# Optimization experiments

Hardware: AMD Instinct MI355X
Metric: run time of the kernel (lower is better)

The kernel has to match this reference:

```python
import jax, jax.numpy as jnp
import numpy as np

NW1, L1 = 4096, 36
NW2, L2 = 1024, 100
D, NHEAD = 128, 8
HD = D // NHEAD
# alternating full / half-full windows -> exact token count
N1 = (NW1 // 2) * (L1 + L1 // 2)   # 110592
N2 = (NW2 // 2) * (L2 + L2 // 2)   # 76800
N = N1 + N2                        # 187392


def _build_group(nw, L, perm, start):
    """Prefix-valid windows: even windows full (L tokens), odd half (L//2)."""
    lens = np.where(np.arange(nw) % 2 == 0, L, L // 2)
    valid = np.arange(L)[None, :] < lens[:, None]          # [nw, L]
    inds = np.zeros((nw, L), np.int32)
    n = int(lens.sum())
    inds[valid] = perm[start:start + n]                    # row-major prefix fill
    return inds, ~valid, start + n


def setup_inputs() -> dict:
    rng = np.random.default_rng(0)
    perm = rng.permutation(N).astype(np.int32)
    inds1, mask1, ptr = _build_group(NW1, L1, perm, 0)
    inds2, mask2, ptr = _build_group(NW2, L2, perm, ptr)
    assert ptr == N
    ks = jax.random.split(jax.random.key(0), 7)
    scale = 1.0 / np.sqrt(D)
    return {
        "feat_2d": jax.random.normal(ks[0], (N, D), jnp.float32),
        "pos1": jax.random.normal(ks[1], (NW1, L1, D), jnp.float32),
        "pos2": jax.random.normal(ks[2], (NW2, L2, D), jnp.float32),
        "in_proj_w": jax.random.normal(ks[3], (3 * D, D), jnp.float32) * scale,
        "in_proj_b": jax.random.normal(ks[4], (3 * D,), jnp.float32) * 0.02,
        "out_proj_w": jax.random.normal(ks[5], (D, D), jnp.float32) * scale,
        "out_proj_b": jax.random.normal(ks[6], (D,), jnp.float32) * 0.02,
        "inds1": jnp.asarray(inds1),
        "inds2": jnp.asarray(inds2),
        "mask1": jnp.asarray(mask1),
        "mask2": jnp.asarray(mask2),
    }


def _mha(qk, v, pad_mask, Wi, bi, Wo, bo):
    """torch.nn.MultiheadAttention math (eval mode, dropout=0).
    qk, v: [nw, L, D]; pad_mask: [nw, L] True=padded key."""
    nw, L, _ = qk.shape
    q = (qk @ Wi[:D].T + bi[:D]).reshape(nw, L, NHEAD, HD)
    k = (qk @ Wi[D:2 * D].T + bi[D:2 * D]).reshape(nw, L, NHEAD, HD)
    vv = (v @ Wi[2 * D:].T + bi[2 * D:]).reshape(nw, L, NHEAD, HD)
    scores = jnp.einsum('nqhd,nkhd->nhqk', q, k) * (HD ** -0.5)
    scores = jnp.where(pad_mask[:, None, None, :],
                       jnp.finfo(scores.dtype).min, scores)
    attn = jax.nn.softmax(scores, axis=-1)
    out = jnp.einsum('nhqk,nkhd->nqhd', attn, vv).reshape(nw, L, D)
    return out @ Wo.T + bo


def reference(feat_2d, pos1, pos2, in_proj_w, in_proj_b, out_proj_w,
              out_proj_b, inds1, inds2, mask1, mask2):
    out = jnp.zeros_like(feat_2d)
    for inds, mask, pos in ((inds1, mask1, pos1), (inds2, mask2, pos2)):
        f = feat_2d[inds]                      # flat2window gather [nw, L, D]
        o = _mha(f + pos, f, mask,
                 in_proj_w, in_proj_b, out_proj_w, out_proj_b)
        o = o * (~mask)[..., None]             # zero padded slots
        out = out.at[inds.reshape(-1)].add(o.reshape(-1, D))  # window2flat
    return out
```

## Files before the change

### kernel.cpp

```cpp
#include <hip/hip_runtime.h>

typedef __attribute__((ext_vector_type(4))) float f32x4;
typedef __attribute__((ext_vector_type(8))) short short8;
typedef __attribute__((ext_vector_type(4))) short short4v;

#define MFMA_B16(a,b,c) __builtin_amdgcn_mfma_f32_16x16x32_bf16((a),(b),(c),0,0,0)

static __device__ __forceinline__ unsigned short f2bf(float x){
  unsigned int u = __float_as_uint(x);
  u += 0x7fffu + ((u >> 16) & 1u);
  return (unsigned short)(u >> 16);
}

static __device__ __forceinline__ short8 pack8(f32x4 a, f32x4 b){
  short8 r;
  r[0]=(short)f2bf(a[0]); r[1]=(short)f2bf(a[1]); r[2]=(short)f2bf(a[2]); r[3]=(short)f2bf(a[3]);
  r[4]=(short)f2bf(b[0]); r[5]=(short)f2bf(b[1]); r[6]=(short)f2bf(b[2]); r[7]=(short)f2bf(b[3]);
  return r;
}

static __device__ __forceinline__ short4v pack4(const f32x4& a){
  short4v r;
  r[0]=(short)f2bf(a[0]); r[1]=(short)f2bf(a[1]); r[2]=(short)f2bf(a[2]); r[3]=(short)f2bf(a[3]);
  return r;
}

__global__ void prep_w(const float* __restrict__ ipw, const float* __restrict__ opw,
                       unsigned short* __restrict__ wbf){
  int i = blockIdx.x * 256 + threadIdx.x;
  float v = (i < 384*128) ? ipw[i] : opw[i - 384*128];
  wbf[i] = f2bf(v);
}

#define STR 136

#define PSTR2 (16*8 + 8)
#define STRT2 24
#define KOFF2 (16*7)

#define TT3 3
#define PSTR3 (16*(TT3+1) + 8)
#define STRT3 24
#define KOFF3 (16*TT3)
#define HALF3 (2*48*STR + 4*16*PSTR3 + 4*16*STRT3)

__global__ __launch_bounds__(512, 4)
void fused_all(const float* __restrict__ feat,
               const float* __restrict__ pos1, const float* __restrict__ pos2,
               const int* __restrict__ inds1, const int* __restrict__ inds2,
               const unsigned short* __restrict__ wqkv,
               const unsigned short* __restrict__ wout,
               const float* __restrict__ ipb, const float* __restrict__ opb,
               float* __restrict__ out)
{
  extern __shared__ __align__(16) unsigned short smem[];
  const int b  = blockIdx.x;
  const int tid = threadIdx.x;
  const short8 Z8 = {0,0,0,0,0,0,0,0};
  const f32x4  Z4 = {0.f,0.f,0.f,0.f};

  if (b < 1024){
    unsigned short* sQK = smem;
    unsigned short* sF  = smem + 112*STR;
    unsigned short* sPb = smem + 2*112*STR;
    unsigned short* sTs = sPb + 4*16*PSTR2;

    const int w  = b;
    const int Lv = (w & 1) ? 50 : 100;
    const int T  = (Lv + 15) >> 4;
    const long ibase = (long)w * 100;
    const int wv4 = tid >> 6, lane = tid & 63, c = lane & 15, q = lane >> 4;

    {
      const int rg = tid >> 4, ch = tid & 15;
      #pragma unroll
      for (int s = 0; s < 4; ++s){
        const int row = s*32 + rg;
        if (row < 16*T){
          short8 fv = Z8, qv = Z8;
          if (row < Lv){
            const int tok = inds2[ibase + row];
            const float* fr = feat + (long)tok*128 + ch*8;
            const float* pr = pos2 + (ibase + row)*128 + ch*8;
            f32x4 f0 = *(const f32x4*)fr, f1 = *(const f32x4*)(fr+4);
            f32x4 p0 = *(const f32x4*)pr, p1 = *(const f32x4*)(pr+4);
            fv = pack8(f0, f1); qv = pack8(f0+p0, f1+p1);
          }
          *(short8*)&sF [row*STR + ch*8] = fv;
          *(short8*)&sQK[row*STR + ch*8] = qv;
        }
      }
    }
    __syncthreads();

    short4v of[2][7];
    if (wv4 < 4){
      const int wv = wv4;
      unsigned short* Pb = sPb + wv*16*PSTR2;
      unsigned short* Ts = sTs + wv*16*STRT2;

      #pragma unroll
      for (int hh = 0; hh < 2; ++hh){
        const int h = wv*2 + hh;
        short8 bQ[4], bK[4], bV[4];
        const unsigned short* wr = wqkv + (h*16 + c)*128 + q*8;
        #pragma unroll
        for (int kk = 0; kk < 4; ++kk){
          bQ[kk] = *(const short8*)(wr + kk*32);
          bK[kk] = *(const short8*)(wr + kk*32 + 128*128);
          bV[kk] = *(const short8*)(wr + kk*32 + 2*128*128);
        }
        float bq_r[4], bk_r[4];
        #pragma unroll
        for (int r = 0; r < 4; ++r){
          bq_r[r] = ipb[h*16 + 4*q + r];
          bk_r[r] = ipb[128 + h*16 + 4*q + r];
        }
        const float bv_c = ipb[256 + h*16 + c];

        short8 qAf[7], kBf[7];

        #pragma unroll
        for (int t = 0; t < 7; ++t) if (t < T){
          f32x4 qt = Z4, kt = Z4, vt = Z4;
          #pragma unroll
          for (int kk = 0; kk < 4; ++kk){
            const short8 aQ = *(const short8*)&sQK[(16*t + c)*STR + kk*32 + q*8];
            const short8 aF = *(const short8*)&sF [(16*t + c)*STR + kk*32 + q*8];
            qt = MFMA_B16(bQ[kk], aQ, qt);
            kt = MFMA_B16(bK[kk], aQ, kt);
            vt = MFMA_B16(aF, bV[kk], vt);
          }
          #pragma unroll
          for (int r = 0; r < 4; ++r){
            qt[r] = (qt[r] + bq_r[r]) * 0.25f;
            kt[r] += bk_r[r];
            const int key = 16*t + 4*q + r;
            vt[r] = (key < Lv) ? (vt[r] + bv_c) : 0.f;
          }
          *(short4v*)&Pb[c*PSTR2 + 16*t + 4*q]   = pack4(vt);
          *(short4v*)&Ts[c*STRT2 + 4*q]          = pack4(qt);
          *(short4v*)&Pb[c*PSTR2 + KOFF2 + 4*q]  = pack4(kt);
          const short8 qf = *(const short8*)&Ts[c*STRT2 + q*8];
          const short8 kf = *(const short8*)&Pb[c*PSTR2 + KOFF2 + q*8];
          qAf[t] = (q < 2) ? qf : Z8;
          kBf[t] = (q < 2) ? kf : Z8;
        }
        {
          const short4v z4 = {0,0,0,0};
          *(short4v*)&Pb[c*PSTR2 + KOFF2 + 4*q] = z4;
        }

        short8 vBf[4];
        #pragma unroll
        for (int u = 0; u < 4; ++u) if (u < ((T+1)>>1))
          vBf[u] = *(const short8*)&Pb[c*PSTR2 + 32*u + q*8];

        #pragma unroll
        for (int t = 0; t < 7; ++t) if (t < T){
          f32x4 St[7];
          #pragma unroll
          for (int tk = 0; tk < 7; ++tk) if (tk < T){
            St[tk] = MFMA_B16(kBf[tk], qAf[t], Z4);
            #pragma unroll
            for (int r = 0; r < 4; ++r){
              const int key = 16*tk + 4*q + r;
              if (key >= Lv) St[tk][r] = -1e30f;
            }
          }
          f32x4 mm = {-1e30f,-1e30f,-1e30f,-1e30f};
          #pragma unroll
          for (int tk = 0; tk < 7; ++tk) if (tk < T){
            mm[0]=fmaxf(mm[0],St[tk][0]); mm[1]=fmaxf(mm[1],St[tk][1]);
            mm[2]=fmaxf(mm[2],St[tk][2]); mm[3]=fmaxf(mm[3],St[tk][3]);
          }
          float m = fmaxf(fmaxf(mm[0],mm[1]), fmaxf(mm[2],mm[3]));
          m = fmaxf(m, __shfl_xor(m, 16));
          m = fmaxf(m, __shfl_xor(m, 32));
          f32x4 ss = Z4;
          #pragma unroll
          for (int tk = 0; tk < 7; ++tk) if (tk < T){
            #pragma unroll
            for (int r = 0; r < 4; ++r){
              float e = __expf(St[tk][r] - m);
              St[tk][r] = e; ss[r] += e;
            }
          }
          float sum = (ss[0]+ss[1]) + (ss[2]+ss[3]);
          sum += __shfl_xor(sum, 16);
          sum += __shfl_xor(sum, 32);
          const float inv = 1.0f / sum;
          #pragma unroll
          for (int tk = 0; tk < 7; ++tk) if (tk < T){
            short4v p4;
            #pragma unroll
            for (int r = 0; r < 4; ++r) p4[r] = (short)f2bf(St[tk][r] * inv);
            *(short4v*)&Pb[c*PSTR2 + 16*tk + 4*q] = p4;
          }
          f32x4 o = Z4;
          #pragma unroll
          for (int u = 0; u < 4; ++u) if (u < ((T+1)>>1)){
            const short8 ap = *(const short8*)&Pb[c*PSTR2 + 32*u + q*8];
            o = MFMA_B16(ap, vBf[u], o);
          }
          short4v ob;
          #pragma unroll
          for (int r = 0; r < 4; ++r) ob[r] = (short)f2bf(o[r]);
          of[hh][t] = ob;
        }
      }
    }

    __syncthreads();
    if (wv4 < 4){
      const int wv = wv4;
      #pragma unroll
      for (int hh = 0; hh < 2; ++hh){
        const int h = wv*2 + hh;
        #pragma unroll
        for (int t = 0; t < 7; ++t) if (t < T){
          #pragma unroll
          for (int r = 0; r < 4; ++r)
            sF[(16*t + 4*q + r)*STR + h*16 + c] = (unsigned short)of[hh][t][r];
        }
      }
    }
    __syncthreads();

    {
      const int t = wv4;
      if (t < T){
        float bo_r[8];
        #pragma unroll
        for (int ct = 0; ct < 8; ++ct) bo_r[ct] = opb[ct*16 + c];
        f32x4 acc[8];
        #pragma unroll
        for (int ct = 0; ct < 8; ++ct) acc[ct] = Z4;
        #pragma unroll
        for (int p = 0; p < 4; ++p){
          const short8 ao = *(const short8*)&sF[(16*t + c)*STR + p*32 + q*8];
          #pragma unroll
          for (int ct = 0; ct < 8; ++ct){
            const short8 bw = *(const short8*)&wout[(ct*16 + c)*128 + p*32 + q*8];
            acc[ct] = MFMA_B16(ao, bw, acc[ct]);
          }
        }
        #pragma unroll
        for (int r = 0; r < 4; ++r){
          const int l = 16*t + 4*q + r;
          if (l < Lv){
            const int tok = inds2[ibase + l];
            float* orow = out + (long)tok*128;
            #pragma unroll
            for (int ct = 0; ct < 8; ++ct)
              orow[ct*16 + c] = acc[ct][r] + bo_r[ct];
          }
        }
      }
    }
  } else {
    const int wv8 = tid >> 6;
    const int wh  = wv8 >> 2;
    const int wv  = wv8 & 3;
    const int lane = tid & 63, c = lane & 15, q = lane >> 4;

    unsigned short* base = smem + wh*HALF3;
    unsigned short* sQK = base;
    unsigned short* sF  = base + 48*STR;
    unsigned short* sPb = base + 2*48*STR;
    unsigned short* sTs = sPb + 4*16*PSTR3;

    const int w = (b - 1024)*2 + wh;
    const int LW = 36;
    const int Lv = wh ? 18 : 36;
    const int T  = wh ? 2 : 3;
    const long ibase = (long)w * LW;

    {
      const int ltid = tid & 255;
      const int rg = ltid >> 4, ch = ltid & 15;
      #pragma unroll
      for (int s = 0; s < TT3; ++s){
        if (s < T){
          const int row = s*16 + rg;
          short8 fv = Z8, qv = Z8;
          if (row < Lv){
            const int tok = inds1[ibase + row];
            const float* fr = feat + (long)tok*128 + ch*8;
            const float* pr = pos1 + (ibase + row)*128 + ch*8;
            f32x4 f0 = *(const f32x4*)fr, f1 = *(const f32x4*)(fr+4);
            f32x4 p0 = *(const f32x4*)pr, p1 = *(const f32x4*)(pr+4);
            fv = pack8(f0, f1); qv = pack8(f0+p0, f1+p1);
          }
          *(short8*)&sF [row*STR + ch*8] = fv;
          *(short8*)&sQK[row*STR + ch*8] = qv;
        }
      }
    }
    __syncthreads();

    unsigned short* Pb = sPb + wv*16*PSTR3;
    unsigned short* Ts = sTs + wv*16*STRT3;
    short4v of[2][TT3];

    #pragma unroll
    for (int hh = 0; hh < 2; ++hh){
      const int h = wv*2 + hh;
      short8 bQ[4], bK[4], bV[4];
      const unsigned short* wr = wqkv + (h*16 + c)*128 + q*8;
      #pragma unroll
      for (int kk = 0; kk < 4; ++kk){
        bQ[kk] = *(const short8*)(wr + kk*32);
        bK[kk] = *(const short8*)(wr + kk*32 + 128*128);
        bV[kk] = *(const short8*)(wr + kk*32 + 2*128*128);
      }
      float bq_r[4], bk_r[4];
      #pragma unroll
      for (int r = 0; r < 4; ++r){
        bq_r[r] = ipb[h*16 + 4*q + r];
        bk_r[r] = ipb[128 + h*16 + 4*q + r];
      }
      const float bv_c = ipb[256 + h*16 + c];

      short8 qAf[TT3], kBf[TT3];

      #pragma unroll
      for (int t = 0; t < TT3; ++t) if (t < T){
        f32x4 qt = Z4, kt = Z4, vt = Z4;
        #pragma unroll
        for (int kk = 0; kk < 4; ++kk){
          const short8 aQ = *(const short8*)&sQK[(16*t + c)*STR + kk*32 + q*8];
          const short8 aF = *(const short8*)&sF [(16*t + c)*STR + kk*32 + q*8];
          qt = MFMA_B16(bQ[kk], aQ, qt);
          kt = MFMA_B16(bK[kk], aQ, kt);
          vt = MFMA_B16(aF, bV[kk], vt);
        }
        #pragma unroll
        for (int r = 0; r < 4; ++r){
          qt[r] = (qt[r] + bq_r[r]) * 0.25f;
          kt[r] += bk_r[r];
          const int key = 16*t + 4*q + r;
          vt[r] = (key < Lv) ? (vt[r] + bv_c) : 0.f;
        }
        *(short4v*)&Pb[c*PSTR3 + 16*t + 4*q]   = pack4(vt);
        *(short4v*)&Ts[c*STRT3 + 4*q]          = pack4(qt);
        *(short4v*)&Pb[c*PSTR3 + KOFF3 + 4*q]  = pack4(kt);
        const short8 qf = *(const short8*)&Ts[c*STRT3 + q*8];
        const short8 kf = *(const short8*)&Pb[c*PSTR3 + KOFF3 + q*8];
        qAf[t] = (q < 2) ? qf : Z8;
        kBf[t] = (q < 2) ? kf : Z8;
      }
      {
        const short4v z4 = {0,0,0,0};
        *(short4v*)&Pb[c*PSTR3 + KOFF3 + 4*q] = z4;
      }

      short8 vBf[2];
      #pragma unroll
      for (int u = 0; u < 2; ++u) if (u < ((T+1)>>1))
        vBf[u] = *(const short8*)&Pb[c*PSTR3 + 32*u + q*8];

      #pragma unroll
      for (int t = 0; t < TT3; ++t) if (t < T){
        f32x4 St[TT3];
        #pragma unroll
        for (int tk = 0; tk < TT3; ++tk) if (tk < T){
          St[tk] = MFMA_B16(kBf[tk], qAf[t], Z4);
          #pragma unroll
          for (int r = 0; r < 4; ++r){
            const int key = 16*tk + 4*q + r;
            if (key >= Lv) St[tk][r] = -1e30f;
          }
        }
        f32x4 mm = {-1e30f,-1e30f,-1e30f,-1e30f};
        #pragma unroll
        for (int tk = 0; tk < TT3; ++tk) if (tk < T){
          mm[0]=fmaxf(mm[0],St[tk][0]); mm[1]=fmaxf(mm[1],St[tk][1]);
          mm[2]=fmaxf(mm[2],St[tk][2]); mm[3]=fmaxf(mm[3],St[tk][3]);
        }
        float m = fmaxf(fmaxf(mm[0],mm[1]), fmaxf(mm[2],mm[3]));
        m = fmaxf(m, __shfl_xor(m, 16));
        m = fmaxf(m, __shfl_xor(m, 32));
        f32x4 ss = Z4;
        #pragma unroll
        for (int tk = 0; tk < TT3; ++tk) if (tk < T){
          #pragma unroll
          for (int r = 0; r < 4; ++r){
            float e = __expf(St[tk][r] - m);
            St[tk][r] = e; ss[r] += e;
          }
        }
        float sum = (ss[0]+ss[1]) + (ss[2]+ss[3]);
        sum += __shfl_xor(sum, 16);
        sum += __shfl_xor(sum, 32);
        const float inv = 1.0f / sum;
        #pragma unroll
        for (int tk = 0; tk < TT3; ++tk) if (tk < T){
          short4v p4;
          #pragma unroll
          for (int r = 0; r < 4; ++r) p4[r] = (short)f2bf(St[tk][r] * inv);
          *(short4v*)&Pb[c*PSTR3 + 16*tk + 4*q] = p4;
        }
        f32x4 o = Z4;
        #pragma unroll
        for (int u = 0; u < 2; ++u) if (u < ((T+1)>>1)){
          const short8 ap = *(const short8*)&Pb[c*PSTR3 + 32*u + q*8];
          o = MFMA_B16(ap, vBf[u], o);
        }
        short4v ob;
        #pragma unroll
        for (int r = 0; r < 4; ++r) ob[r] = (short)f2bf(o[r]);
        of[hh][t] = ob;
      }
    }

    __syncthreads();
    #pragma unroll
    for (int hh = 0; hh < 2; ++hh){
      const int h = wv*2 + hh;
      #pragma unroll
      for (int t = 0; t < TT3; ++t) if (t < T){
        #pragma unroll
        for (int r = 0; r < 4; ++r)
          sF[(16*t + 4*q + r)*STR + h*16 + c] = (unsigned short)of[hh][t][r];
      }
    }
    __syncthreads();

    {
      const int t = wv;
      if (t < T){
        float bo_r[8];
        #pragma unroll
        for (int ct = 0; ct < 8; ++ct) bo_r[ct] = opb[ct*16 + c];
        f32x4 acc[8];
        #pragma unroll
        for (int ct = 0; ct < 8; ++ct) acc[ct] = Z4;
        #pragma unroll
        for (int p = 0; p < 4; ++p){
          const short8 ao = *(const short8*)&sF[(16*t + c)*STR + p*32 + q*8];
          #pragma unroll
          for (int ct = 0; ct < 8; ++ct){
            const short8 bw = *(const short8*)&wout[(ct*16 + c)*128 + p*32 + q*8];
            acc[ct] = MFMA_B16(ao, bw, acc[ct]);
          }
        }
        #pragma unroll
        for (int r = 0; r < 4; ++r){
          const int l = 16*t + 4*q + r;
          if (l < Lv){
            const int tok = inds1[ibase + l];
            float* orow = out + (long)tok*128;
            #pragma unroll
            for (int ct = 0; ct < 8; ++ct)
              orow[ct*16 + c] = acc[ct][r] + bo_r[ct];
          }
        }
      }
    }
  }
}

extern "C" void kernel_launch(void* const* d_in, const int* in_sizes, int n_in,
                              void* d_out, int out_size, void* d_ws, size_t ws_size,
                              hipStream_t stream) {
  const float* feat = (const float*)d_in[0];
  const float* pos1 = (const float*)d_in[1];
  const float* pos2 = (const float*)d_in[2];
  const float* ipw  = (const float*)d_in[3];
  const float* ipb  = (const float*)d_in[4];
  const float* opw  = (const float*)d_in[5];
  const float* opb  = (const float*)d_in[6];
  const int*   inds1 = (const int*)d_in[7];
  const int*   inds2 = (const int*)d_in[8];
  float* out = (float*)d_out;
  unsigned short* wbf = (unsigned short*)d_ws;
  unsigned short* wob = wbf + 384*128;

  prep_w<<<dim3(256), dim3(256), 0, stream>>>(ipw, opw, wbf);

  const int lds = (2*112*STR + 4*16*PSTR2 + 4*16*STRT2) * 2;
  hipFuncSetAttribute((const void*)fused_all,
                      hipFuncAttributeMaxDynamicSharedMemorySize, lds);
  fused_all<<<dim3(1024 + 2048), dim3(512), lds, stream>>>(
      feat, pos1, pos2, inds1, inds2, wbf, wob, ipb, opb, out);
}
```

Before: 435.0 us.

## Use all eight waves for L=100 windows, one head per wave

```diff
diff --git a/kernel.cpp b/kernel.cpp
--- a/kernel.cpp
+++ b/kernel.cpp
@@ -36,7 +36,6 @@
 
 #define PSTR2 (16*8 + 8)
 #define STRT2 24
-#define KOFF2 (16*7)
 
 #define TT3 3
 #define PSTR3 (16*(TT3+1) + 8)
@@ -62,14 +61,14 @@
   if (b < 1024){
     unsigned short* sQK = smem;
     unsigned short* sF  = smem + 112*STR;
-    unsigned short* sPb = smem + 2*112*STR;
-    unsigned short* sTs = sPb + 4*16*PSTR2;
+    unsigned short* sTs = smem + 2*112*STR;
+    unsigned short* sPx = sTs + 8*16*STRT2;
 
     const int w  = b;
     const int Lv = (w & 1) ? 50 : 100;
     const int T  = (Lv + 15) >> 4;
     const long ibase = (long)w * 100;
-    const int wv4 = tid >> 6, lane = tid & 63, c = lane & 15, q = lane >> 4;
+    const int wv8 = tid >> 6, lane = tid & 63, c = lane & 15, q = lane >> 4;
 
     {
       const int rg = tid >> 4, ch = tid & 15;
@@ -93,142 +92,145 @@
     }
     __syncthreads();
 
-    short4v of[2][7];
-    if (wv4 < 4){
-      const int wv = wv4;
-      unsigned short* Pb = sPb + wv*16*PSTR2;
-      unsigned short* Ts = sTs + wv*16*STRT2;
-
-      #pragma unroll
-      for (int hh = 0; hh < 2; ++hh){
-        const int h = wv*2 + hh;
-        short8 bQ[4], bK[4], bV[4];
-        const unsigned short* wr = wqkv + (h*16 + c)*128 + q*8;
+    const int h = wv8;
+    unsigned short* Ts = sTs + wv8*16*STRT2;
+    short8 qAf[7], kBf[7];
+
+    {
+      short8 bQ[4], bK[4];
+      const unsigned short* wr = wqkv + (h*16 + c)*128 + q*8;
+      #pragma unroll
+      for (int kk = 0; kk < 4; ++kk){
+        bQ[kk] = *(const short8*)(wr + kk*32);
+        bK[kk] = *(const short8*)(wr + kk*32 + 128*128);
+      }
+      float bq_r[4], bk_r[4];
+      #pragma unroll
+      for (int r = 0; r < 4; ++r){
+        bq_r[r] = ipb[h*16 + 4*q + r];
+        bk_r[r] = ipb[128 + h*16 + 4*q + r];
+      }
+      #pragma unroll
+      for (int t = 0; t < 7; ++t) if (t < T){
+        f32x4 qt = Z4, kt = Z4;
         #pragma unroll
         for (int kk = 0; kk < 4; ++kk){
-          bQ[kk] = *(const short8*)(wr + kk*32);
-          bK[kk] = *(const short8*)(wr + kk*32 + 128*128);
-          bV[kk] = *(const short8*)(wr + kk*32 + 2*128*128);
-        }
-        float bq_r[4], bk_r[4];
-        #pragma unroll
-        for (int r = 0; r < 4; ++r){
-          bq_r[r] = ipb[h*16 + 4*q + r];
-          bk_r[r] = ipb[128 + h*16 + 4*q + r];
-        }
-        const float bv_c = ipb[256 + h*16 + c];
-
-        short8 qAf[7], kBf[7];
-
-        #pragma unroll
-        for (int t = 0; t < 7; ++t) if (t < T){
-          f32x4 qt = Z4, kt = Z4, vt = Z4;
-          #pragma unroll
-          for (int kk = 0; kk < 4; ++kk){
-            const short8 aQ = *(const short8*)&sQK[(16*t + c)*STR + kk*32 + q*8];
-            const short8 aF = *(const short8*)&sF [(16*t + c)*STR + kk*32 + q*8];
-            qt = MFMA_B16(bQ[kk], aQ, qt);
-            kt = MFMA_B16(bK[kk], aQ, kt);
-            vt = MFMA_B16(aF, bV[kk], vt);
-          }
-          #pragma unroll
-          for (int r = 0; r < 4; ++r){
-            qt[r] = (qt[r] + bq_r[r]) * 0.25f;
-            kt[r] += bk_r[r];
-            const int key = 16*t + 4*q + r;
-            vt[r] = (key < Lv) ? (vt[r] + bv_c) : 0.f;
-          }
-          *(short4v*)&Pb[c*PSTR2 + 16*t + 4*q]   = pack4(vt);
-          *(short4v*)&Ts[c*STRT2 + 4*q]          = pack4(qt);
-          *(short4v*)&Pb[c*PSTR2 + KOFF2 + 4*q]  = pack4(kt);
-          const short8 qf = *(const short8*)&Ts[c*STRT2 + q*8];
-          const short8 kf = *(const short8*)&Pb[c*PSTR2 + KOFF2 + q*8];
-          qAf[t] = (q < 2) ? qf : Z8;
-          kBf[t] = (q < 2) ? kf : Z8;
-        }
-        {
-          const short4v z4 = {0,0,0,0};
-          *(short4v*)&Pb[c*PSTR2 + KOFF2 + 4*q] = z4;
-        }
-
-        short8 vBf[4];
-        #pragma unroll
-        for (int u = 0; u < 4; ++u) if (u < ((T+1)>>1))
-          vBf[u] = *(const short8*)&Pb[c*PSTR2 + 32*u + q*8];
-
-        #pragma unroll
-        for (int t = 0; t < 7; ++t) if (t < T){
-          f32x4 St[7];
-          #pragma unroll
-          for (int tk = 0; tk < 7; ++tk) if (tk < T){
-            St[tk] = MFMA_B16(kBf[tk], qAf[t], Z4);
-            #pragma unroll
-            for (int r = 0; r < 4; ++r){
-              const int key = 16*tk + 4*q + r;
-              if (key >= Lv) St[tk][r] = -1e30f;
-            }
-          }
-          f32x4 mm = {-1e30f,-1e30f,-1e30f,-1e30f};
-          #pragma unroll
-          for (int tk = 0; tk < 7; ++tk) if (tk < T){
-            mm[0]=fmaxf(mm[0],St[tk][0]); mm[1]=fmaxf(mm[1],St[tk][1]);
-            mm[2]=fmaxf(mm[2],St[tk][2]); mm[3]=fmaxf(mm[3],St[tk][3]);
-          }
-          float m = fmaxf(fmaxf(mm[0],mm[1]), fmaxf(mm[2],mm[3]));
-          m = fmaxf(m, __shfl_xor(m, 16));
-          m = fmaxf(m, __shfl_xor(m, 32));
-          f32x4 ss = Z4;
-          #pragma unroll
-          for (int tk = 0; tk < 7; ++tk) if (tk < T){
-            #pragma unroll
-            for (int r = 0; r < 4; ++r){
-              float e = __expf(St[tk][r] - m);
-              St[tk][r] = e; ss[r] += e;
-            }
-          }
-          float sum = (ss[0]+ss[1]) + (ss[2]+ss[3]);
-          sum += __shfl_xor(sum, 16);
-          sum += __shfl_xor(sum, 32);
-          const float inv = 1.0f / sum;
-          #pragma unroll
-          for (int tk = 0; tk < 7; ++tk) if (tk < T){
-            short4v p4;
-            #pragma unroll
-            for (int r = 0; r < 4; ++r) p4[r] = (short)f2bf(St[tk][r] * inv);
-            *(short4v*)&Pb[c*PSTR2 + 16*tk + 4*q] = p4;
-          }
-          f32x4 o = Z4;
-          #pragma unroll
-          for (int u = 0; u < 4; ++u) if (u < ((T+1)>>1)){
-            const short8 ap = *(const short8*)&Pb[c*PSTR2 + 32*u + q*8];
-            o = MFMA_B16(ap, vBf[u], o);
-          }
-          short4v ob;
-          #pragma unroll
-          for (int r = 0; r < 4; ++r) ob[r] = (short)f2bf(o[r]);
-          of[hh][t] = ob;
-        }
-      }
-    }
-
-    __syncthreads();
-    if (wv4 < 4){
-      const int wv = wv4;
-      #pragma unroll
-      for (int hh = 0; hh < 2; ++hh){
-        const int h = wv*2 + hh;
-        #pragma unroll
-        for (int t = 0; t < 7; ++t) if (t < T){
-          #pragma unroll
-          for (int r = 0; r < 4; ++r)
-            sF[(16*t + 4*q + r)*STR + h*16 + c] = (unsigned short)of[hh][t][r];
-        }
-      }
-    }
-    __syncthreads();
-
-    {
-      const int t = wv4;
+          const short8 aQ = *(const short8*)&sQK[(16*t + c)*STR + kk*32 + q*8];
+          qt = MFMA_B16(bQ[kk], aQ, qt);
+          kt = MFMA_B16(bK[kk], aQ, kt);
+        }
+        #pragma unroll
+        for (int r = 0; r < 4; ++r){
+          qt[r] = (qt[r] + bq_r[r]) * 0.25f;
+          kt[r] += bk_r[r];
+        }
+        *(short4v*)&Ts[c*STRT2 + 4*q] = pack4(qt);
+        const short8 qf = *(const short8*)&Ts[c*STRT2 + q*8];
+        qAf[t] = (q < 2) ? qf : Z8;
+        *(short4v*)&Ts[c*STRT2 + 4*q] = pack4(kt);
+        const short8 kf = *(const short8*)&Ts[c*STRT2 + q*8];
+        kBf[t] = (q < 2) ? kf : Z8;
+      }
+    }
+    __syncthreads();
+
+    unsigned short* Pb = (wv8 < 7) ? (smem + wv8*16*PSTR2) : sPx;
+
+    {
+      short8 bV[4];
+      const unsigned short* wr = wqkv + (h*16 + c)*128 + q*8 + 2*128*128;
+      #pragma unroll
+      for (int kk = 0; kk < 4; ++kk) bV[kk] = *(const short8*)(wr + kk*32);
+      const float bv_c = ipb[256 + h*16 + c];
+      #pragma unroll
+      for (int t = 0; t < 7; ++t) if (t < T){
+        f32x4 vt = Z4;
+        #pragma unroll
+        for (int kk = 0; kk < 4; ++kk){
+          const short8 aF = *(const short8*)&sF[(16*t + c)*STR + kk*32 + q*8];
+          vt = MFMA_B16(aF, bV[kk], vt);
+        }
+        #pragma unroll
+        for (int r = 0; r < 4; ++r){
+          const int key = 16*t + 4*q + r;
+          vt[r] = (key < Lv) ? (vt[r] + bv_c) : 0.f;
+        }
+        *(short4v*)&Pb[c*PSTR2 + 16*t + 4*q] = pack4(vt);
+      }
+      const short4v z4 = {0,0,0,0};
+      *(short4v*)&Pb[c*PSTR2 + 112 + 4*q] = z4;
+    }
+
+    short8 vBf[4];
+    #pragma unroll
+    for (int u = 0; u < 4; ++u) if (u < ((T+1)>>1))
+      vBf[u] = *(const short8*)&Pb[c*PSTR2 + 32*u + q*8];
+
+    short4v of[7];
+    #pragma unroll
+    for (int t = 0; t < 7; ++t) if (t < T){
+      f32x4 St[7];
+      #pragma unroll
+      for (int tk = 0; tk < 7; ++tk) if (tk < T){
+        St[tk] = MFMA_B16(kBf[tk], qAf[t], Z4);
+        #pragma unroll
+        for (int r = 0; r < 4; ++r){
+          const int key = 16*tk + 4*q + r;
+          if (key >= Lv) St[tk][r] = -1e30f;
+        }
+      }
+      f32x4 mm = {-1e30f,-1e30f,-1e30f,-1e30f};
+      #pragma unroll
+      for (int tk = 0; tk < 7; ++tk) if (tk < T){
+        mm[0]=fmaxf(mm[0],St[tk][0]); mm[1]=fmaxf(mm[1],St[tk][1]);
+        mm[2]=fmaxf(mm[2],St[tk][2]); mm[3]=fmaxf(mm[3],St[tk][3]);
+      }
+      float m = fmaxf(fmaxf(mm[0],mm[1]), fmaxf(mm[2],mm[3]));
+      m = fmaxf(m, __shfl_xor(m, 16));
+      m = fmaxf(m, __shfl_xor(m, 32));
+      f32x4 ss = Z4;
+      #pragma unroll
+      for (int tk = 0; tk < 7; ++tk) if (tk < T){
+        #pragma unroll
+        for (int r = 0; r < 4; ++r){
+          float e = __expf(St[tk][r] - m);
+          St[tk][r] = e; ss[r] += e;
+        }
+      }
+      float sum = (ss[0]+ss[1]) + (ss[2]+ss[3]);
+      sum += __shfl_xor(sum, 16);
+      sum += __shfl_xor(sum, 32);
+      const float inv = 1.0f / sum;
+      #pragma unroll
+      for (int tk = 0; tk < 7; ++tk) if (tk < T){
+        short4v p4;
+        #pragma unroll
+        for (int r = 0; r < 4; ++r) p4[r] = (short)f2bf(St[tk][r] * inv);
+        *(short4v*)&Pb[c*PSTR2 + 16*tk + 4*q] = p4;
+      }
+      f32x4 o = Z4;
+      #pragma unroll
+      for (int u = 0; u < 4; ++u) if (u < ((T+1)>>1)){
+        const short8 ap = *(const short8*)&Pb[c*PSTR2 + 32*u + q*8];
+        o = MFMA_B16(ap, vBf[u], o);
+      }
+      short4v ob;
+      #pragma unroll
+      for (int r = 0; r < 4; ++r) ob[r] = (short)f2bf(o[r]);
+      of[t] = ob;
+    }
+
+    __syncthreads();
+    #pragma unroll
+    for (int t = 0; t < 7; ++t) if (t < T){
+      #pragma unroll
+      for (int r = 0; r < 4; ++r)
+        sF[(16*t + 4*q + r)*STR + h*16 + c] = (unsigned short)of[t][r];
+    }
+    __syncthreads();
+
+    {
+      const int t = wv8;
       if (t < T){
         float bo_r[8];
         #pragma unroll
@@ -479,7 +481,7 @@
 
   prep_w<<<dim3(256), dim3(256), 0, stream>>>(ipw, opw, wbf);
 
-  const int lds = (2*112*STR + 4*16*PSTR2 + 4*16*STRT2) * 2;
+  const int lds = 2*HALF3*2;
   hipFuncSetAttribute((const void*)fused_all,
                       hipFuncAttributeMaxDynamicSharedMemorySize, lds);
   fused_all<<<dim3(1024 + 2048), dim3(512), lds, stream>>>(
```

New measurement: 405.0 us. 6.9% less time.
